# Kernel optimization log

Hardware: AMD Instinct MI355X
Metric: run time of the kernel (lower is better)

The kernel has to match this reference:

```python
import jax, jax.numpy as jnp
import numpy as np

EDGE_TYPES = 7
TIME_STEP = 5
STATE_DIM = 1024


def setup_inputs() -> dict:
    key = jax.random.key(0)
    ks = jax.random.split(key, 8)
    B, T, N, DF = 4, 15, 15, 25600
    S, E = STATE_DIM, EDGE_TYPES
    # weights ~ N(0, 0.01), biases zero, matching _initialization()
    return {
        "pose_features": jax.random.normal(ks[0], (B, T, N, DF), jnp.float32),
        "W_compress": jax.random.normal(ks[1], (DF, S), jnp.float32) * 0.01,
        "b_compress": jnp.zeros((S,), jnp.float32),
        "W_edge": jax.random.normal(ks[2], (E, S, S), jnp.float32) * 0.01,
        "b_edge": jnp.zeros((E, S), jnp.float32),
        "W_att": jax.random.normal(ks[3], (E, 2 * S), jnp.float32) * 0.01,
        "b_att": jnp.zeros((E,), jnp.float32),
        "W_r": jax.random.normal(ks[4], (2 * S, S), jnp.float32) * 0.01,
        "b_r": jnp.zeros((S,), jnp.float32),
        "W_z": jax.random.normal(ks[5], (2 * S, S), jnp.float32) * 0.01,
        "b_z": jnp.zeros((S,), jnp.float32),
        "W_h": jax.random.normal(ks[6], (2 * S, S), jnp.float32) * 0.01,
        "b_h": jnp.zeros((S,), jnp.float32),
    }


def reference(pose_features, W_compress, b_compress, W_edge, b_edge,
              W_att, b_att, W_r, b_r, W_z, b_z, W_h, b_h):
    B, T, N, DF = pose_features.shape
    S = W_compress.shape[1]
    E = W_edge.shape[0]
    x = pose_features.reshape(B * T, N, DF)
    prop = x @ W_compress + b_compress                      # [M, N, S]
    # attention Linear over concat(row, col) == row-part + col-part (rank-1 broadcast,
    # avoids materializing the [M, N, N, 2S] repeat/cat tensor; identical math)
    Wa_row, Wa_col = W_att[:, :S], W_att[:, S:]
    scores = None
    for _ in range(1 + TIME_STEP):
        msg = jnp.einsum('bnd,edh->benh', prop, W_edge) + b_edge[None, :, None, :]  # [M,E,N,S]
        row = jnp.einsum('bend,ed->ben', msg, Wa_row)       # [M, E, N]
        col = jnp.einsum('bend,ed->ben', msg, Wa_col)
        scores = jax.nn.sigmoid(row[..., :, None] + col[..., None, :]
                                + b_att[None, :, None, None])   # [M, E, N, N]
        merged = jnp.einsum('beij,bejd->bid', scores, msg)  # [M, N, S]
        a = jnp.concatenate([merged, prop], axis=-1)        # [M, N, 2S]
        r = jax.nn.sigmoid(a @ W_r + b_r)
        z = jax.nn.sigmoid(a @ W_z + b_z)
        h_hat = jnp.tanh(jnp.concatenate([merged, r * prop], axis=-1) @ W_h + b_h)
        prop = (1 - z) * prop + z * h_hat
    box_states = scores.transpose(0, 2, 3, 1)               # [M, N, N, E]
    action_score = ((1 - box_states[..., 0:1]) * box_states).sum(axis=2)
    action_score = action_score.reshape(B, T, N, E)
    actor_score = (1 - box_states[..., 0]).reshape(B, T, N, N)
    acty_score = jax.nn.softmax(
        (action_score * actor_score.sum(axis=-1)[..., None]).sum(axis=2)[:, :, 1:],
        axis=-1)
    return action_score, acty_score, actor_score
```

## Files before the change

### kernel.cpp

```cpp
#include <hip/hip_runtime.h>
#include <hip/hip_bf16.h>

typedef unsigned short bf16_t;
typedef __bf16 bf16x8 __attribute__((ext_vector_type(8)));
typedef float f32x4 __attribute__((ext_vector_type(4)));
typedef unsigned short ushort8_t __attribute__((ext_vector_type(8)));

__device__ __forceinline__ unsigned short f2bf(float x){
  union { __hip_bfloat16 h; unsigned short u; } c;
  c.h = __float2bfloat16(x);
  return c.u;
}
__device__ __forceinline__ float bf2f(bf16_t u){
  union { unsigned short u; __hip_bfloat16 h; } c;
  c.u = u;
  return __bfloat162float(c.h);
}

template<int ACT, int MAP>
__global__ __launch_bounds__(256, 2)
void gemm_bf16(const bf16_t* __restrict__ A, int lda,
               const bf16_t* __restrict__ Bt, int ldb,
               float* __restrict__ C, int ldc, size_t csplit,
               const float* __restrict__ bias,
               int M, int N, int K, int Kchunk)
{
  __shared__ __align__(16) bf16_t As[2][128*64];
  __shared__ __align__(16) bf16_t Bs[2][128*64];
  const int tid = threadIdx.x;
  const int w = tid >> 6, lane = tid & 63;
  const int wm = w >> 1, wn = w & 1;
  const int lr = lane & 15, kq = lane >> 4;
  int bcol, brow, bks;
  if (MAP == 0) { bcol = blockIdx.x; brow = blockIdx.y; bks = blockIdx.z; }
  else          { bks = blockIdx.x;  bcol = blockIdx.y; brow = blockIdx.z; }
  const int gm0 = brow * 128, gn0 = bcol * 128;
  const int k0 = bks * Kchunk;
  const int nt = (min(k0 + Kchunk, K) - k0) >> 6;

  const bf16_t *pA0, *pA1, *pA2, *pA3, *pB0, *pB1, *pB2, *pB3;
  {
    const int u0 = tid, r_0 = u0 >> 3, g0 = (u0 & 7) ^ (r_0 & 7);
    const int u1 = tid + 256, r_1 = u1 >> 3, g1 = (u1 & 7) ^ (r_1 & 7);
    const int u2 = tid + 512, r_2 = u2 >> 3, g2 = (u2 & 7) ^ (r_2 & 7);
    const int u3 = tid + 768, r_3 = u3 >> 3, g3 = (u3 & 7) ^ (r_3 & 7);
    pA0 = A + (size_t)min(gm0 + r_0, M-1)*lda + k0 + g0*8;
    pA1 = A + (size_t)min(gm0 + r_1, M-1)*lda + k0 + g1*8;
    pA2 = A + (size_t)min(gm0 + r_2, M-1)*lda + k0 + g2*8;
    pA3 = A + (size_t)min(gm0 + r_3, M-1)*lda + k0 + g3*8;
    pB0 = Bt + (size_t)min(gn0 + r_0, N-1)*ldb + k0 + g0*8;
    pB1 = Bt + (size_t)min(gn0 + r_1, N-1)*ldb + k0 + g1*8;
    pB2 = Bt + (size_t)min(gn0 + r_2, N-1)*ldb + k0 + g2*8;
    pB3 = Bt + (size_t)min(gn0 + r_3, N-1)*ldb + k0 + g3*8;
  }
  bf16_t* Al = &As[0][0] + tid*8;
  bf16_t* Bl = &Bs[0][0] + tid*8;
  ushort8_t va0, va1, va2, va3, vb0, vb1, vb2, vb3;

#define LDT(t) do { \
    va0 = *(const ushort8_t*)(pA0 + (size_t)(t)*64); \
    va1 = *(const ushort8_t*)(pA1 + (size_t)(t)*64); \
    va2 = *(const ushort8_t*)(pA2 + (size_t)(t)*64); \
    va3 = *(const ushort8_t*)(pA3 + (size_t)(t)*64); \
    vb0 = *(const ushort8_t*)(pB0 + (size_t)(t)*64); \
    vb1 = *(const ushort8_t*)(pB1 + (size_t)(t)*64); \
    vb2 = *(const ushort8_t*)(pB2 + (size_t)(t)*64); \
    vb3 = *(const ushort8_t*)(pB3 + (size_t)(t)*64); \
  } while(0)
#define WRT(b) do { \
    *(ushort8_t*)(Al + (b)*8192)        = va0; \
    *(ushort8_t*)(Al + (b)*8192 + 2048) = va1; \
    *(ushort8_t*)(Al + (b)*8192 + 4096) = va2; \
    *(ushort8_t*)(Al + (b)*8192 + 6144) = va3; \
    *(ushort8_t*)(Bl + (b)*8192)        = vb0; \
    *(ushort8_t*)(Bl + (b)*8192 + 2048) = vb1; \
    *(ushort8_t*)(Bl + (b)*8192 + 4096) = vb2; \
    *(ushort8_t*)(Bl + (b)*8192 + 6144) = vb3; } while(0)

  LDT(0); WRT(0);
  if (nt > 1) LDT(1);
  asm volatile("s_waitcnt lgkmcnt(0)" ::: "memory");
  __builtin_amdgcn_s_barrier();
  __builtin_amdgcn_sched_barrier(0);

  const int ph = lr & 7;
  f32x4 acc[4][4] = {};

  for (int t = 0; t < nt; ++t) {
    const int cb = t & 1;
    const bf16_t* Ab = &As[0][0] + cb*8192;
    const bf16_t* Bb = &Bs[0][0] + cb*8192;
    bf16x8 af[2][4], bfr[2][4];
#pragma unroll
    for (int ks = 0; ks < 2; ks++) {
      const int phys = (ks*4 + kq) ^ ph;
#pragma unroll
      for (int mi = 0; mi < 4; mi++)
        af[ks][mi] = *(const bf16x8*)(Ab + (wm*64 + mi*16 + lr)*64 + phys*8);
#pragma unroll
      for (int ni = 0; ni < 4; ni++)
        bfr[ks][ni] = *(const bf16x8*)(Bb + (wn*64 + ni*16 + lr)*64 + phys*8);
    }
    if (t + 1 < nt) WRT(cb ^ 1);
    if (t + 2 < nt) LDT(t + 2);
    __builtin_amdgcn_s_setprio(1);
#pragma unroll
    for (int ks = 0; ks < 2; ks++)
#pragma unroll
      for (int mi = 0; mi < 4; mi++)
#pragma unroll
        for (int ni = 0; ni < 4; ni++)
          acc[mi][ni] = __builtin_amdgcn_mfma_f32_16x16x32_bf16(af[ks][mi], bfr[ks][ni], acc[mi][ni], 0, 0, 0);
    __builtin_amdgcn_s_setprio(0);
    asm volatile("s_waitcnt lgkmcnt(0)" ::: "memory");
    __builtin_amdgcn_s_barrier();
    __builtin_amdgcn_sched_barrier(0);
  }
#undef LDT
#undef WRT

#pragma unroll
  for (int mi = 0; mi < 4; mi++) {
#pragma unroll
    for (int ni = 0; ni < 4; ni++) {
      const int col = gn0 + wn*64 + ni*16 + lr;
      const float bv = (ACT == 4) ? bias[col] : 0.f;
#pragma unroll
      for (int i = 0; i < 4; i++) {
        const int row = gm0 + wm*64 + mi*16 + kq*4 + i;
        if (row < M) {
          const float v = acc[mi][ni][i] + bv;
          if (ACT == 4) ((bf16_t*)C)[(size_t)row*ldc + col] = f2bf(v);
          else C[(size_t)bks*csplit + (size_t)row*ldc + col] = v;
        }
      }
    }
  }
}

__global__ void reduce_compress(const float* __restrict__ part, const float* __restrict__ bias,
                                float* __restrict__ prop, bf16_t* __restrict__ xr)
{
  const int idx = blockIdx.x*256 + threadIdx.x;
  const int m = idx >> 10, d = idx & 1023;
  float v = bias[d];
#pragma unroll
  for (int z = 0; z < 8; z++) v += part[(size_t)z*921600 + idx];
  prop[idx] = v;
  xr[(size_t)m*2048 + 1024 + d] = f2bf(v);
}

__global__ void reduce_rz(const float* __restrict__ part, const float* __restrict__ bias,
                          const float* __restrict__ prop, float* __restrict__ Zbuf,
                          bf16_t* __restrict__ Xh)
{
  const int idx = blockIdx.x*256 + threadIdx.x;
  const int m = idx >> 11, c = idx & 2047;
  float v = part[idx] + part[1843200 + idx] + bias[c];
  v = 1.f / (1.f + __expf(-v));
  if (c < 1024) Xh[(size_t)m*2048 + 1024 + c] = f2bf(v * prop[(size_t)m*1024 + c]);
  else          Zbuf[(size_t)m*1024 + (c - 1024)] = v;
}

__global__ void reduce_h(const float* __restrict__ part, const float* __restrict__ bias,
                         const float* __restrict__ Zbuf, float* __restrict__ prop,
                         bf16_t* __restrict__ X)
{
  const int idx = blockIdx.x*256 + threadIdx.x;
  const int m = idx >> 10, d = idx & 1023;
  float v = bias[d];
#pragma unroll
  for (int z = 0; z < 4; z++) v += part[(size_t)z*921600 + idx];
  v = tanhf(v);
  const float zz = Zbuf[idx];
  const float pn = (1.f - zz)*prop[idx] + zz*v;
  prop[idx] = pn;
  X[(size_t)m*2048 + 1024 + d] = f2bf(pn);
}

__global__ void compute_u(const float* __restrict__ We, const float* __restrict__ Wa,
                          float* __restrict__ u_row, float* __restrict__ u_col)
{
  const int w = threadIdx.x >> 6, lane = threadIdx.x & 63;
  const int idx = blockIdx.x*4 + w;
  const int e = idx >> 10, h = idx & 1023;
  const float* wep = We + ((size_t)e*1024 + h)*1024;
  const float* wr  = Wa + (size_t)e*2048;
  const float* wc  = wr + 1024;
  float ar = 0.f, ac = 0.f;
#pragma unroll
  for (int t = 0; t < 16; t++) {
    const float v = wep[lane + 64*t];
    ar += v*wr[lane + 64*t];
    ac += v*wc[lane + 64*t];
  }
  for (int off = 32; off; off >>= 1) { ar += __shfl_down(ar, off); ac += __shfl_down(ac, off); }
  if (lane == 0) { u_row[idx] = ar; u_col[idx] = ac; }
}

__global__ void crc_kernel(const float* __restrict__ be, const float* __restrict__ Wa,
                           float* __restrict__ crc)
{
  const int w = threadIdx.x >> 6, lane = threadIdx.x & 63;
  for (int idx = w; idx < 14; idx += 4) {
    const int e = idx >> 1, which = idx & 1;
    const float* bp = be + e*1024;
    const float* wp = Wa + (size_t)e*2048 + which*1024;
    float a = 0.f;
#pragma unroll
    for (int t = 0; t < 16; t++) a += bp[lane + 64*t]*wp[lane + 64*t];
    for (int off = 32; off; off >>= 1) a += __shfl_down(a, off);
    if (lane == 0) crc[which*7 + e] = a;
  }
}

__global__ void attn_kernel(const float* __restrict__ prop, const float* __restrict__ u_row,
                            const float* __restrict__ u_col, const float* __restrict__ crc,
                            const float* __restrict__ b_att, float* __restrict__ scores)
{
  const int b = blockIdx.x, e = blockIdx.y;
  __shared__ float rowv[15], colv[15];
  const int w = threadIdx.x >> 6, lane = threadIdx.x & 63;
  const float* ur = u_row + (size_t)e*1024;
  const float* uc = u_col + (size_t)e*1024;
  for (int n = w; n < 15; n += 4) {
    const float* pr = prop + (size_t)(b*15 + n)*1024;
    float ar = 0.f, ac = 0.f;
#pragma unroll
    for (int t = 0; t < 16; t++) {
      const float pv = pr[lane + 64*t];
      ar += pv*ur[lane + 64*t];
      ac += pv*uc[lane + 64*t];
    }
    for (int off = 32; off; off >>= 1) { ar += __shfl_down(ar, off); ac += __shfl_down(ac, off); }
    if (lane == 0) { rowv[n] = ar; colv[n] = ac; }
  }
  __syncthreads();
  const float base = b_att[e] + crc[e] + crc[7 + e];
  for (int idx = threadIdx.x; idx < 225; idx += 256) {
    const int i = idx/15, j = idx - i*15;
    const float s = 1.f / (1.f + __expf(-(rowv[i] + colv[j] + base)));
    scores[((size_t)(b*7 + e)*15 + i)*15 + j] = s;
  }
}

__global__ void merged_kernel(const bf16_t* __restrict__ msg, const float* __restrict__ scores,
                              bf16_t* __restrict__ X, bf16_t* __restrict__ Xh)
{
  const int b = blockIdx.x, c = blockIdx.y;
  __shared__ float ms[15*7*128];
  __shared__ float sc[1575];
  for (int q = threadIdx.x; q < 3360; q += 256) {
    const int idx = q*4;
    const int j = idx / 896;
    const int rem = idx - j*896;
    const int e = rem >> 7, dl = rem & 127;
    const ushort4 v = *(const ushort4*)(msg + (size_t)(b*15 + j)*7168 + e*1024 + c*128 + dl);
    ms[idx]   = bf2f(v.x);
    ms[idx+1] = bf2f(v.y);
    ms[idx+2] = bf2f(v.z);
    ms[idx+3] = bf2f(v.w);
  }
  for (int idx = threadIdx.x; idx < 1575; idx += 256)
    sc[idx] = scores[(size_t)b*1575 + idx];
  __syncthreads();
  for (int oi = threadIdx.x; oi < 1920; oi += 256) {
    const int i = oi >> 7, dl = oi & 127;
    float acc = 0.f;
#pragma unroll
    for (int e = 0; e < 7; e++)
#pragma unroll
      for (int j = 0; j < 15; j++)
        acc += sc[(e*15 + i)*15 + j] * ms[j*896 + e*128 + dl];
    const bf16_t o = f2bf(acc);
    X [(size_t)(b*15 + i)*2048 + c*128 + dl] = o;
    Xh[(size_t)(b*15 + i)*2048 + c*128 + dl] = o;
  }
}

__global__ void transpose_k(const float* __restrict__ in, bf16_t* __restrict__ out,
                            int R, int C, int out_ld, size_t in_batch, size_t out_batch)
{
  __shared__ float t[64][65];
  in  += (size_t)blockIdx.z * in_batch;
  out += (size_t)blockIdx.z * out_batch;
  const int r0 = blockIdx.x*64, c0 = blockIdx.y*64;
  const int tc = threadIdx.x & 63, tr = threadIdx.x >> 6;
#pragma unroll
  for (int i = 0; i < 16; i++) {
    const int r = tr*16 + i;
    t[r][tc] = in[(size_t)(r0 + r)*C + c0 + tc];
  }
  __syncthreads();
#pragma unroll
  for (int i = 0; i < 16; i++) {
    const int rr = tr*16 + i;
    out[(size_t)(c0 + rr)*out_ld + r0 + tc] = f2bf(t[tc][rr]);
  }
}

__global__ void cast_f32_bf16(const float4* __restrict__ in, ushort4* __restrict__ out, int n4)
{
  int i = blockIdx.x*256 + threadIdx.x;
  const int stride = gridDim.x*256;
  for (; i < n4; i += stride) {
    const float4 v = in[i];
    out[i] = make_ushort4(f2bf(v.x), f2bf(v.y), f2bf(v.z), f2bf(v.w));
  }
}

__global__ void cat2_kernel(const float* __restrict__ a, const float* __restrict__ b,
                            float* __restrict__ o)
{
  const int i = blockIdx.x*256 + threadIdx.x;
  if (i < 1024) o[i] = a[i];
  else if (i < 2048) o[i] = b[i - 1024];
}

__global__ void finalize_kernel(const float* __restrict__ scores, float* __restrict__ out)
{
  const int b = blockIdx.x;
  __shared__ float sc[1575];
  __shared__ float act[105];
  __shared__ float asum[15];
  __shared__ float t2[7];
  for (int idx = threadIdx.x; idx < 1575; idx += 256)
    sc[idx] = scores[(size_t)b*1575 + idx];
  __syncthreads();
  for (int idx = threadIdx.x; idx < 105; idx += 256) {
    const int i = idx/7, e = idx - i*7;
    float a = 0.f;
#pragma unroll
    for (int j = 0; j < 15; j++)
      a += (1.f - sc[i*15 + j]) * sc[(e*15 + i)*15 + j];
    act[idx] = a;
    out[(size_t)b*105 + idx] = a;
  }
  for (int idx = threadIdx.x; idx < 225; idx += 256) {
    const int i = idx/15, j = idx - i*15;
    out[6660 + (size_t)b*225 + idx] = 1.f - sc[i*15 + j];
  }
  if (threadIdx.x < 15) {
    const int i = threadIdx.x;
    float s = 0.f;
#pragma unroll
    for (int j = 0; j < 15; j++) s += 1.f - sc[i*15 + j];
    asum[i] = s;
  }
  __syncthreads();
  if (threadIdx.x < 7) {
    const int e = threadIdx.x;
    float t = 0.f;
#pragma unroll
    for (int i = 0; i < 15; i++) t += act[i*7 + e]*asum[i];
    t2[e] = t;
  }
  __syncthreads();
  if (threadIdx.x == 0) {
    float mx = -1e30f;
    for (int e = 1; e < 7; e++) mx = fmaxf(mx, t2[e]);
    float s = 0.f, ex[6];
    for (int e = 1; e < 7; e++) { ex[e-1] = __expf(t2[e] - mx); s += ex[e-1]; }
    for (int e = 1; e < 7; e++) out[6300 + (size_t)b*6 + (e-1)] = ex[e-1]/s;
  }
}

extern "C" void kernel_launch(void* const* d_in, const int* in_sizes, int n_in,
                              void* d_out, int out_size, void* d_ws, size_t ws_size,
                              hipStream_t stream)
{
  const float* pose = (const float*)d_in[0];
  const float* Wc   = (const float*)d_in[1];
  const float* bc   = (const float*)d_in[2];
  const float* We   = (const float*)d_in[3];
  const float* be   = (const float*)d_in[4];
  const float* Wa   = (const float*)d_in[5];
  const float* ba   = (const float*)d_in[6];
  const float* Wr   = (const float*)d_in[7];
  const float* br   = (const float*)d_in[8];
  const float* Wz   = (const float*)d_in[9];
  const float* bz   = (const float*)d_in[10];
  const float* Wh   = (const float*)d_in[11];
  const float* bh   = (const float*)d_in[12];
  float* out = (float*)d_out;

  char* p = (char*)d_ws;
  auto alloc = [&](size_t b) { char* r = p; p += (b + 255) & ~(size_t)255; return r; };
  bf16_t* Wedge_t = (bf16_t*)alloc(7168ull*1024*2);
  bf16_t* Wrz_t   = (bf16_t*)alloc(2048ull*2048*2);
  bf16_t* Wh_t    = (bf16_t*)alloc(1024ull*2048*2);
  bf16_t* X       = (bf16_t*)alloc(900ull*2048*2);
  float*  prop    = (float*) alloc(900ull*1024*4);
  float*  scores  = (float*) alloc(60ull*7*15*15*4);
  float*  u_row   = (float*) alloc(7168*4);
  float*  u_col   = (float*) alloc(7168*4);
  float*  crc     = (float*) alloc(64);
  float*  brzv    = (float*) alloc(2048*4);
  char* r1 = alloc(128000000ull);
  bf16_t* Abf     = (bf16_t*)r1;
  bf16_t* Wct     = (bf16_t*)(r1 + 46080000ull);
  float*  partial = (float*) (r1 + 46080000ull + 52428800ull);
  bf16_t* msgb    = (bf16_t*)r1;
  float*  Zbuf    = (float*) (r1 + 12902400ull);
  bf16_t* Xh      = (bf16_t*)(r1 + 16588800ull);
  float*  partRZ  = (float*) (r1 + 20275200ull);
  float*  partH   = (float*) (r1 + 49766400ull);

  compute_u<<<1792, 256, 0, stream>>>(We, Wa, u_row, u_col);
  crc_kernel<<<1, 256, 0, stream>>>(be, Wa, crc);
  cast_f32_bf16<<<2048, 256, 0, stream>>>((const float4*)pose, (ushort4*)Abf, 23040000/4);
  transpose_k<<<dim3(400,16,1), 256, 0, stream>>>(Wc, Wct, 25600, 1024, 25600, 0, 0);
  transpose_k<<<dim3(16,16,7),  256, 0, stream>>>(We, Wedge_t, 1024, 1024, 1024,
                                                  1024ull*1024, 1024ull*1024);
  transpose_k<<<dim3(32,16,1),  256, 0, stream>>>(Wr, Wrz_t, 2048, 1024, 2048, 0, 0);
  transpose_k<<<dim3(32,16,1),  256, 0, stream>>>(Wz, Wrz_t + 1024ull*2048, 2048, 1024, 2048, 0, 0);
  transpose_k<<<dim3(32,16,1),  256, 0, stream>>>(Wh, Wh_t, 2048, 1024, 2048, 0, 0);
  cat2_kernel<<<8, 256, 0, stream>>>(br, bz, brzv);

  gemm_bf16<0,1><<<dim3(8,8,8), 256, 0, stream>>>(Abf, 25600, Wct, 25600,
      partial, 1024, 921600ull, nullptr, 900, 1024, 25600, 3200);
  reduce_compress<<<3600, 256, 0, stream>>>(partial, bc, prop, X);

  for (int it = 0; it < 6; it++) {
    attn_kernel<<<dim3(60,7), 256, 0, stream>>>(prop, u_row, u_col, crc, ba, scores);
    if (it == 5) break;
    gemm_bf16<4,0><<<dim3(56,8,1), 256, 0, stream>>>(X + 1024, 2048, Wedge_t, 1024,
        (float*)msgb, 7168, 0, be, 900, 7168, 1024, 1024);
    merged_kernel<<<dim3(60,8), 256, 0, stream>>>(msgb, scores, X, Xh);
    gemm_bf16<0,0><<<dim3(16,8,2), 256, 0, stream>>>(X, 2048, Wrz_t, 2048,
        partRZ, 2048, 1843200ull, nullptr, 900, 2048, 2048, 1024);
    reduce_rz<<<7200, 256, 0, stream>>>(partRZ, brzv, prop, Zbuf, Xh);
    gemm_bf16<0,0><<<dim3(8,8,4), 256, 0, stream>>>(Xh, 2048, Wh_t, 2048,
        partH, 1024, 921600ull, nullptr, 900, 1024, 2048, 512);
    reduce_h<<<3600, 256, 0, stream>>>(partH, bh, Zbuf, prop, X);
  }

  finalize_kernel<<<60, 256, 0, stream>>>(scores, out);
}
```

Measured before the change: 641.2 us.

## Pre-pack weight B-fragments and load them directly into registers, bypassing LDS

Replaces the weight transposes with a packing kernel that lays out each weight matrix in MFMA B-fragment order, 512 bf16 per 16-column by 32-k tile. The GEMM now reads B fragments straight from global memory into registers with double buffering, and only A goes through shared memory. This halves LDS traffic and footprint per block and removes the B LDS writes and reads. In exchange, B loads become per-wave global loads with no reuse across waves in the block, and the register count goes up.

Result: slower. 1.424 ms (+122.1%).

```diff
diff --git a/kernel.cpp b/kernel.cpp
--- a/kernel.cpp
+++ b/kernel.cpp
@@ -19,14 +19,13 @@
 
 template<int ACT, int MAP>
 __global__ __launch_bounds__(256, 2)
-void gemm_bf16(const bf16_t* __restrict__ A, int lda,
-               const bf16_t* __restrict__ Bt, int ldb,
-               float* __restrict__ C, int ldc, size_t csplit,
-               const float* __restrict__ bias,
-               int M, int N, int K, int Kchunk)
+void gemm_hyb(const bf16_t* __restrict__ A, int lda,
+              const bf16_t* __restrict__ Bpk, int KTB,
+              float* __restrict__ C, int ldc, size_t csplit,
+              const float* __restrict__ bias,
+              int M, int Kchunk)
 {
   __shared__ __align__(16) bf16_t As[2][128*64];
-  __shared__ __align__(16) bf16_t Bs[2][128*64];
   const int tid = threadIdx.x;
   const int w = tid >> 6, lane = tid & 63;
   const int wm = w >> 1, wn = w & 1;
@@ -36,73 +35,70 @@
   else          { bks = blockIdx.x;  bcol = blockIdx.y; brow = blockIdx.z; }
   const int gm0 = brow * 128, gn0 = bcol * 128;
   const int k0 = bks * Kchunk;
-  const int nt = (min(k0 + Kchunk, K) - k0) >> 6;
-
-  const bf16_t *pA0, *pA1, *pA2, *pA3, *pB0, *pB1, *pB2, *pB3;
+  const int nt = Kchunk >> 6;
+  const int ksB = bks * (Kchunk >> 5);
+
+  const bf16_t *pA0, *pA1, *pA2, *pA3;
   {
-    const int u0 = tid, r_0 = u0 >> 3, g0 = (u0 & 7) ^ (r_0 & 7);
-    const int u1 = tid + 256, r_1 = u1 >> 3, g1 = (u1 & 7) ^ (r_1 & 7);
-    const int u2 = tid + 512, r_2 = u2 >> 3, g2 = (u2 & 7) ^ (r_2 & 7);
-    const int u3 = tid + 768, r_3 = u3 >> 3, g3 = (u3 & 7) ^ (r_3 & 7);
-    pA0 = A + (size_t)min(gm0 + r_0, M-1)*lda + k0 + g0*8;
-    pA1 = A + (size_t)min(gm0 + r_1, M-1)*lda + k0 + g1*8;
-    pA2 = A + (size_t)min(gm0 + r_2, M-1)*lda + k0 + g2*8;
-    pA3 = A + (size_t)min(gm0 + r_3, M-1)*lda + k0 + g3*8;
-    pB0 = Bt + (size_t)min(gn0 + r_0, N-1)*ldb + k0 + g0*8;
-    pB1 = Bt + (size_t)min(gn0 + r_1, N-1)*ldb + k0 + g1*8;
-    pB2 = Bt + (size_t)min(gn0 + r_2, N-1)*ldb + k0 + g2*8;
-    pB3 = Bt + (size_t)min(gn0 + r_3, N-1)*ldb + k0 + g3*8;
+    const int u0 = tid,       r0 = u0 >> 3, g0 = (u0 & 7) ^ (r0 & 7);
+    const int u1 = tid + 256, r1 = u1 >> 3, g1 = (u1 & 7) ^ (r1 & 7);
+    const int u2 = tid + 512, r2 = u2 >> 3, g2 = (u2 & 7) ^ (r2 & 7);
+    const int u3 = tid + 768, r3 = u3 >> 3, g3 = (u3 & 7) ^ (r3 & 7);
+    pA0 = A + (size_t)min(gm0 + r0, M-1)*lda + k0 + g0*8;
+    pA1 = A + (size_t)min(gm0 + r1, M-1)*lda + k0 + g1*8;
+    pA2 = A + (size_t)min(gm0 + r2, M-1)*lda + k0 + g2*8;
+    pA3 = A + (size_t)min(gm0 + r3, M-1)*lda + k0 + g3*8;
   }
   bf16_t* Al = &As[0][0] + tid*8;
-  bf16_t* Bl = &Bs[0][0] + tid*8;
-  ushort8_t va0, va1, va2, va3, vb0, vb1, vb2, vb3;
-
-#define LDT(t) do { \
+  ushort8_t va0, va1, va2, va3;
+
+  const bf16_t* pb[4];
+#pragma unroll
+  for (int q = 0; q < 4; q++)
+    pb[q] = Bpk + ((size_t)(bcol*8 + wn*4 + q)*KTB + ksB)*512 + lane*8;
+
+  bf16x8 b[2][8];
+  f32x4 acc[4][4] = {};
+
+#define LDA(t) do { \
     va0 = *(const ushort8_t*)(pA0 + (size_t)(t)*64); \
     va1 = *(const ushort8_t*)(pA1 + (size_t)(t)*64); \
     va2 = *(const ushort8_t*)(pA2 + (size_t)(t)*64); \
     va3 = *(const ushort8_t*)(pA3 + (size_t)(t)*64); \
-    vb0 = *(const ushort8_t*)(pB0 + (size_t)(t)*64); \
-    vb1 = *(const ushort8_t*)(pB1 + (size_t)(t)*64); \
-    vb2 = *(const ushort8_t*)(pB2 + (size_t)(t)*64); \
-    vb3 = *(const ushort8_t*)(pB3 + (size_t)(t)*64); \
   } while(0)
-#define WRT(b) do { \
-    *(ushort8_t*)(Al + (b)*8192)        = va0; \
-    *(ushort8_t*)(Al + (b)*8192 + 2048) = va1; \
-    *(ushort8_t*)(Al + (b)*8192 + 4096) = va2; \
-    *(ushort8_t*)(Al + (b)*8192 + 6144) = va3; \
-    *(ushort8_t*)(Bl + (b)*8192)        = vb0; \
-    *(ushort8_t*)(Bl + (b)*8192 + 2048) = vb1; \
-    *(ushort8_t*)(Bl + (b)*8192 + 4096) = vb2; \
-    *(ushort8_t*)(Bl + (b)*8192 + 6144) = vb3; } while(0)
-
-  LDT(0); WRT(0);
-  if (nt > 1) LDT(1);
+#define WRA(bf) do { \
+    *(ushort8_t*)(Al + (bf)*8192)        = va0; \
+    *(ushort8_t*)(Al + (bf)*8192 + 2048) = va1; \
+    *(ushort8_t*)(Al + (bf)*8192 + 4096) = va2; \
+    *(ushort8_t*)(Al + (bf)*8192 + 6144) = va3; } while(0)
+#define LDB(BUF, t) do { \
+    _Pragma("unroll") \
+    for (int q = 0; q < 4; q++) { \
+      b[BUF][q]     = *(const bf16x8*)(pb[q] + (size_t)(t)*1024); \
+      b[BUF][q + 4] = *(const bf16x8*)(pb[q] + (size_t)(t)*1024 + 512); \
+    } } while(0)
+
+  LDA(0); WRA(0);
+  LDB(0, 0);
+  if (nt > 1) { LDB(1, 1); LDA(1); }
   asm volatile("s_waitcnt lgkmcnt(0)" ::: "memory");
   __builtin_amdgcn_s_barrier();
   __builtin_amdgcn_sched_barrier(0);
 
   const int ph = lr & 7;
-  f32x4 acc[4][4] = {};
-
   for (int t = 0; t < nt; ++t) {
     const int cb = t & 1;
     const bf16_t* Ab = &As[0][0] + cb*8192;
-    const bf16_t* Bb = &Bs[0][0] + cb*8192;
-    bf16x8 af[2][4], bfr[2][4];
+    bf16x8 af[2][4];
 #pragma unroll
     for (int ks = 0; ks < 2; ks++) {
       const int phys = (ks*4 + kq) ^ ph;
 #pragma unroll
       for (int mi = 0; mi < 4; mi++)
         af[ks][mi] = *(const bf16x8*)(Ab + (wm*64 + mi*16 + lr)*64 + phys*8);
-#pragma unroll
-      for (int ni = 0; ni < 4; ni++)
-        bfr[ks][ni] = *(const bf16x8*)(Bb + (wn*64 + ni*16 + lr)*64 + phys*8);
     }
-    if (t + 1 < nt) WRT(cb ^ 1);
-    if (t + 2 < nt) LDT(t + 2);
+    if (t + 1 < nt) WRA(cb ^ 1);
+    if (t + 2 < nt) LDA(t + 2);
     __builtin_amdgcn_s_setprio(1);
 #pragma unroll
     for (int ks = 0; ks < 2; ks++)
@@ -110,14 +106,17 @@
       for (int mi = 0; mi < 4; mi++)
 #pragma unroll
         for (int ni = 0; ni < 4; ni++)
-          acc[mi][ni] = __builtin_amdgcn_mfma_f32_16x16x32_bf16(af[ks][mi], bfr[ks][ni], acc[mi][ni], 0, 0, 0);
+          acc[mi][ni] = __builtin_amdgcn_mfma_f32_16x16x32_bf16(
+              af[ks][mi], b[cb][ks*4 + ni], acc[mi][ni], 0, 0, 0);
     __builtin_amdgcn_s_setprio(0);
+    if (t + 2 < nt) LDB(cb, t + 2);
     asm volatile("s_waitcnt lgkmcnt(0)" ::: "memory");
     __builtin_amdgcn_s_barrier();
     __builtin_amdgcn_sched_barrier(0);
   }
-#undef LDT
-#undef WRT
+#undef LDA
+#undef WRA
+#undef LDB
 
 #pragma unroll
   for (int mi = 0; mi < 4; mi++) {
@@ -135,6 +134,30 @@
         }
       }
     }
+  }
+}
+
+__global__ void pack_bfrag(const float* __restrict__ src, bf16_t* __restrict__ dst,
+                           int srcldN, int KT, int n0t, size_t in_batch, int ogb)
+{
+  const int ntb = blockIdx.x, kt = blockIdx.y, bz = blockIdx.z;
+  src += (size_t)bz * in_batch;
+  const int ng0 = n0t + bz*ogb + ntb*8;
+  __shared__ float s[32][132];
+  for (int i = threadIdx.x; i < 4096; i += 256) {
+    const int kl = i >> 7, nl = i & 127;
+    s[kl][nl] = src[(size_t)(kt*32 + kl)*srcldN + ntb*128 + nl];
+  }
+  __syncthreads();
+  for (int u = threadIdx.x; u < 512; u += 256) {
+    const int t = u >> 6, ln = u & 63;
+    const int n = t*16 + (ln & 15), kq = ln >> 4;
+    ushort4 v0, v1;
+    v0 = make_ushort4(f2bf(s[kq*8+0][n]), f2bf(s[kq*8+1][n]), f2bf(s[kq*8+2][n]), f2bf(s[kq*8+3][n]));
+    v1 = make_ushort4(f2bf(s[kq*8+4][n]), f2bf(s[kq*8+5][n]), f2bf(s[kq*8+6][n]), f2bf(s[kq*8+7][n]));
+    bf16_t* dt = dst + ((size_t)(ng0 + t)*KT + kt)*512 + ln*8;
+    *(ushort4*)dt = v0;
+    *(ushort4*)(dt + 4) = v1;
   }
 }
 
@@ -275,27 +298,6 @@
     const bf16_t o = f2bf(acc);
     X [(size_t)(b*15 + i)*2048 + c*128 + dl] = o;
     Xh[(size_t)(b*15 + i)*2048 + c*128 + dl] = o;
-  }
-}
-
-__global__ void transpose_k(const float* __restrict__ in, bf16_t* __restrict__ out,
-                            int R, int C, int out_ld, size_t in_batch, size_t out_batch)
-{
-  __shared__ float t[64][65];
-  in  += (size_t)blockIdx.z * in_batch;
-  out += (size_t)blockIdx.z * out_batch;
-  const int r0 = blockIdx.x*64, c0 = blockIdx.y*64;
-  const int tc = threadIdx.x & 63, tr = threadIdx.x >> 6;
-#pragma unroll
-  for (int i = 0; i < 16; i++) {
-    const int r = tr*16 + i;
-    t[r][tc] = in[(size_t)(r0 + r)*C + c0 + tc];
-  }
-  __syncthreads();
-#pragma unroll
-  for (int i = 0; i < 16; i++) {
-    const int rr = tr*16 + i;
-    out[(size_t)(c0 + rr)*out_ld + r0 + tc] = f2bf(t[tc][rr]);
   }
 }
 
@@ -386,19 +388,19 @@
 
   char* p = (char*)d_ws;
   auto alloc = [&](size_t b) { char* r = p; p += (b + 255) & ~(size_t)255; return r; };
-  bf16_t* Wedge_t = (bf16_t*)alloc(7168ull*1024*2);
-  bf16_t* Wrz_t   = (bf16_t*)alloc(2048ull*2048*2);
-  bf16_t* Wh_t    = (bf16_t*)alloc(1024ull*2048*2);
-  bf16_t* X       = (bf16_t*)alloc(900ull*2048*2);
-  float*  prop    = (float*) alloc(900ull*1024*4);
-  float*  scores  = (float*) alloc(60ull*7*15*15*4);
-  float*  u_row   = (float*) alloc(7168*4);
-  float*  u_col   = (float*) alloc(7168*4);
-  float*  crc     = (float*) alloc(64);
-  float*  brzv    = (float*) alloc(2048*4);
+  bf16_t* Wedgep = (bf16_t*)alloc(448ull*32*1024);
+  bf16_t* Wrzp   = (bf16_t*)alloc(128ull*64*1024);
+  bf16_t* Whp    = (bf16_t*)alloc(64ull*64*1024);
+  bf16_t* X      = (bf16_t*)alloc(900ull*2048*2);
+  float*  prop   = (float*) alloc(900ull*1024*4);
+  float*  scores = (float*) alloc(60ull*7*15*15*4);
+  float*  u_row  = (float*) alloc(7168*4);
+  float*  u_col  = (float*) alloc(7168*4);
+  float*  crc    = (float*) alloc(64);
+  float*  brzv   = (float*) alloc(2048*4);
   char* r1 = alloc(128000000ull);
   bf16_t* Abf     = (bf16_t*)r1;
-  bf16_t* Wct     = (bf16_t*)(r1 + 46080000ull);
+  bf16_t* Wcp     = (bf16_t*)(r1 + 46080000ull);
   float*  partial = (float*) (r1 + 46080000ull + 52428800ull);
   bf16_t* msgb    = (bf16_t*)r1;
   float*  Zbuf    = (float*) (r1 + 12902400ull);
@@ -408,30 +410,30 @@
 
   compute_u<<<1792, 256, 0, stream>>>(We, Wa, u_row, u_col);
   crc_kernel<<<1, 256, 0, stream>>>(be, Wa, crc);
+  cat2_kernel<<<8, 256, 0, stream>>>(br, bz, brzv);
   cast_f32_bf16<<<2048, 256, 0, stream>>>((const float4*)pose, (ushort4*)Abf, 23040000/4);
-  transpose_k<<<dim3(400,16,1), 256, 0, stream>>>(Wc, Wct, 25600, 1024, 25600, 0, 0);
-  transpose_k<<<dim3(16,16,7),  256, 0, stream>>>(We, Wedge_t, 1024, 1024, 1024,
-                                                  1024ull*1024, 1024ull*1024);
-  transpose_k<<<dim3(32,16,1),  256, 0, stream>>>(Wr, Wrz_t, 2048, 1024, 2048, 0, 0);
-  transpose_k<<<dim3(32,16,1),  256, 0, stream>>>(Wz, Wrz_t + 1024ull*2048, 2048, 1024, 2048, 0, 0);
-  transpose_k<<<dim3(32,16,1),  256, 0, stream>>>(Wh, Wh_t, 2048, 1024, 2048, 0, 0);
-  cat2_kernel<<<8, 256, 0, stream>>>(br, bz, brzv);
-
-  gemm_bf16<0,1><<<dim3(8,8,8), 256, 0, stream>>>(Abf, 25600, Wct, 25600,
-      partial, 1024, 921600ull, nullptr, 900, 1024, 25600, 3200);
+  pack_bfrag<<<dim3(8,800), 256, 0, stream>>>(Wc, Wcp, 1024, 800, 0, 0, 0);
+  pack_bfrag<<<dim3(8,32,7), 256, 0, stream>>>(We, Wedgep, 1024, 32, 0,
+                                               1024ull*1024, 64);
+  pack_bfrag<<<dim3(8,64), 256, 0, stream>>>(Wr, Wrzp, 1024, 64, 0, 0, 0);
+  pack_bfrag<<<dim3(8,64), 256, 0, stream>>>(Wz, Wrzp, 1024, 64, 64, 0, 0);
+  pack_bfrag<<<dim3(8,64), 256, 0, stream>>>(Wh, Whp, 1024, 64, 0, 0, 0);
+
+  gemm_hyb<0,1><<<dim3(8,8,8), 256, 0, stream>>>(Abf, 25600, Wcp, 800,
+      partial, 1024, 921600ull, nullptr, 900, 3200);
   reduce_compress<<<3600, 256, 0, stream>>>(partial, bc, prop, X);
 
   for (int it = 0; it < 6; it++) {
     attn_kernel<<<dim3(60,7), 256, 0, stream>>>(prop, u_row, u_col, crc, ba, scores);
     if (it == 5) break;
-    gemm_bf16<4,0><<<dim3(56,8,1), 256, 0, stream>>>(X + 1024, 2048, Wedge_t, 1024,
-        (float*)msgb, 7168, 0, be, 900, 7168, 1024, 1024);
+    gemm_hyb<4,0><<<dim3(56,8,1), 256, 0, stream>>>(X + 1024, 2048, Wedgep, 32,
+        (float*)msgb, 7168, 0, be, 900, 1024);
     merged_kernel<<<dim3(60,8), 256, 0, stream>>>(msgb, scores, X, Xh);
-    gemm_bf16<0,0><<<dim3(16,8,2), 256, 0, stream>>>(X, 2048, Wrz_t, 2048,
-        partRZ, 2048, 1843200ull, nullptr, 900, 2048, 2048, 1024);
+    gemm_hyb<0,0><<<dim3(16,8,2), 256, 0, stream>>>(X, 2048, Wrzp, 64,
+        partRZ, 2048, 1843200ull, nullptr, 900, 1024);
     reduce_rz<<<7200, 256, 0, stream>>>(partRZ, brzv, prop, Zbuf, Xh);
-    gemm_bf16<0,0><<<dim3(8,8,4), 256, 0, stream>>>(Xh, 2048, Wh_t, 2048,
-        partH, 1024, 921600ull, nullptr, 900, 1024, 2048, 512);
+    gemm_hyb<0,0><<<dim3(8,8,4), 256, 0, stream>>>(Xh, 2048, Whp, 64,
+        partH, 1024, 921600ull, nullptr, 900, 512);
     reduce_h<<<3600, 256, 0, stream>>>(partH, bh, Zbuf, prop, X);
   }
 
```
